# Kernel tuning notes

Hardware: AMD Instinct MI355X
Metric: run time of the kernel (lower is better)

The kernel has to match this reference:

```python
import jax, jax.numpy as jnp
import numpy as np

N, V, L = 256, 4, 100000
MUTATION_PROB = 0.2


def setup_inputs() -> dict:
    key = jax.random.key(0)
    k_s, k_mask, k_cat = jax.random.split(key, 3)
    # One-hot encoded input sequences (n, v, l), like the original module expects.
    base = jax.random.randint(k_s, (N, L), 0, V)
    s = jax.nn.one_hot(base, V, axis=1, dtype=jnp.float32)  # (n, v, l)
    # Externalized randomness: bernoulli mutation mask and uniform categorical draws.
    mask = jax.random.bernoulli(k_mask, MUTATION_PROB, (N, L))  # bool (n, l)
    cats = jax.random.randint(k_cat, (N, L), 0, V).astype(jnp.int32)  # (n, l)
    return {"s": s, "mask": mask, "cats": cats}


def reference(s, mask, cats):
    # s: (n, v, l) float; mask: (n, l) bool; cats: (n, l) int in [0, v)
    n, v, l = s.shape
    # One-hot of the sampled categories along the vocab axis -> (n, v, l)
    onehot = jax.nn.one_hot(cats, v, axis=1, dtype=s.dtype)
    # At mutated positions, replace the whole one-hot column with the new sample.
    return jnp.where(mask[:, None, :], onehot, s)
```

## Files before the change

kernel.cpp:

```cpp
#include <hip/hip_runtime.h>


#define N_SEQ 256
#define V_VOCAB 4
#define L_LEN 100000
#define L4 (L_LEN / 4)

__global__ void mutate_kernel(const float* __restrict__ s,
                              const int* __restrict__ mask,
                              const int* __restrict__ cats,
                              float* __restrict__ out) {
    const long long total = (long long)N_SEQ * L4;
    const long long stride = (long long)gridDim.x * blockDim.x;
    for (long long idx = (long long)blockIdx.x * blockDim.x + threadIdx.x;
         idx < total; idx += stride) {
        const int n  = (int)(idx / L4);
        const int lc = (int)(idx % L4);
        const long long nl = (long long)n * L_LEN + (long long)lc * 4;

        const int4 m = *reinterpret_cast<const int4*>(mask + nl);
        const int4 c = *reinterpret_cast<const int4*>(cats + nl);

        #pragma unroll
        for (int v = 0; v < V_VOCAB; ++v) {
            const long long off = ((long long)n * V_VOCAB + v) * L_LEN
                                + (long long)lc * 4;
            const float4 sv = *reinterpret_cast<const float4*>(s + off);
            float4 o;
            o.x = m.x ? (c.x == v ? 1.0f : 0.0f) : sv.x;
            o.y = m.y ? (c.y == v ? 1.0f : 0.0f) : sv.y;
            o.z = m.z ? (c.z == v ? 1.0f : 0.0f) : sv.z;
            o.w = m.w ? (c.w == v ? 1.0f : 0.0f) : sv.w;
            *reinterpret_cast<float4*>(out + off) = o;
        }
    }
}

extern "C" void kernel_launch(void* const* d_in, const int* in_sizes, int n_in,
                              void* d_out, int out_size, void* d_ws, size_t ws_size,
                              hipStream_t stream) {
    const float* s    = (const float*)d_in[0];
    const int*   mask = (const int*)d_in[1];
    const int*   cats = (const int*)d_in[2];
    float* out = (float*)d_out;

    const int block = 256;
    const long long total = (long long)N_SEQ * L4;
    int grid = (int)((total + block - 1) / block);
    if (grid > 2048) grid = 2048;

    mutate_kernel<<<grid, block, 0, stream>>>(s, mask, cats, out);
}
```

Before: 192.5 us.

## Use 2D grid, 8 elements per thread, and nontemporal loads/stores

Replaces the capped grid-stride loop with a 2D grid (chunks by sequence) so there is no per-element 64-bit div/mod. Each thread now handles 8 positions using two 16-byte vectors per stream, and all loads and stores use nontemporal hints to avoid polluting the cache with streaming data. This launches many more blocks and raises per-thread register use. Strided 32-byte per-thread accesses may reduce coalescing efficiency compared to contiguous 16-byte accesses.

Result: no change. 195.0 us (+1.3%).

```diff
diff --git a/kernel.cpp b/kernel.cpp
--- a/kernel.cpp
+++ b/kernel.cpp
@@ -4,35 +4,42 @@
 #define N_SEQ 256
 #define V_VOCAB 4
 #define L_LEN 100000
-#define L4 (L_LEN / 4)
+#define LPT 8
+#define L_CHUNKS (L_LEN / LPT)
 
-__global__ void mutate_kernel(const float* __restrict__ s,
-                              const int* __restrict__ mask,
-                              const int* __restrict__ cats,
-                              float* __restrict__ out) {
-    const long long total = (long long)N_SEQ * L4;
-    const long long stride = (long long)gridDim.x * blockDim.x;
-    for (long long idx = (long long)blockIdx.x * blockDim.x + threadIdx.x;
-         idx < total; idx += stride) {
-        const int n  = (int)(idx / L4);
-        const int lc = (int)(idx % L4);
-        const long long nl = (long long)n * L_LEN + (long long)lc * 4;
+typedef int   vint4   __attribute__((ext_vector_type(4)));
+typedef float vfloat4 __attribute__((ext_vector_type(4)));
 
-        const int4 m = *reinterpret_cast<const int4*>(mask + nl);
-        const int4 c = *reinterpret_cast<const int4*>(cats + nl);
+__global__ __launch_bounds__(256)
+void mutate_kernel(const float* __restrict__ s,
+                   const int* __restrict__ mask,
+                   const int* __restrict__ cats,
+                   float* __restrict__ out) {
+    const int lc = blockIdx.x * blockDim.x + threadIdx.x;
+    if (lc >= L_CHUNKS) return;
+    const int n = blockIdx.y;
 
+    const int l0 = lc * LPT;
+    const long long nl = (long long)n * L_LEN + l0;
+
+    const vint4 m0 = __builtin_nontemporal_load(reinterpret_cast<const vint4*>(mask + nl));
+    const vint4 m1 = __builtin_nontemporal_load(reinterpret_cast<const vint4*>(mask + nl) + 1);
+    const vint4 c0 = __builtin_nontemporal_load(reinterpret_cast<const vint4*>(cats + nl));
+    const vint4 c1 = __builtin_nontemporal_load(reinterpret_cast<const vint4*>(cats + nl) + 1);
+
+    #pragma unroll
+    for (int v = 0; v < V_VOCAB; ++v) {
+        const long long off = ((long long)n * V_VOCAB + v) * L_LEN + l0;
+        const vfloat4 s0 = __builtin_nontemporal_load(reinterpret_cast<const vfloat4*>(s + off));
+        const vfloat4 s1 = __builtin_nontemporal_load(reinterpret_cast<const vfloat4*>(s + off) + 1);
+        vfloat4 o0, o1;
         #pragma unroll
-        for (int v = 0; v < V_VOCAB; ++v) {
-            const long long off = ((long long)n * V_VOCAB + v) * L_LEN
-                                + (long long)lc * 4;
-            const float4 sv = *reinterpret_cast<const float4*>(s + off);
-            float4 o;
-            o.x = m.x ? (c.x == v ? 1.0f : 0.0f) : sv.x;
-            o.y = m.y ? (c.y == v ? 1.0f : 0.0f) : sv.y;
-            o.z = m.z ? (c.z == v ? 1.0f : 0.0f) : sv.z;
-            o.w = m.w ? (c.w == v ? 1.0f : 0.0f) : sv.w;
-            *reinterpret_cast<float4*>(out + off) = o;
+        for (int j = 0; j < 4; ++j) {
+            o0[j] = m0[j] ? (c0[j] == v ? 1.0f : 0.0f) : s0[j];
+            o1[j] = m1[j] ? (c1[j] == v ? 1.0f : 0.0f) : s1[j];
         }
+        __builtin_nontemporal_store(o0, reinterpret_cast<vfloat4*>(out + off));
+        __builtin_nontemporal_store(o1, reinterpret_cast<vfloat4*>(out + off) + 1);
     }
 }
 
@@ -45,9 +52,6 @@
     float* out = (float*)d_out;
 
     const int block = 256;
-    const long long total = (long long)N_SEQ * L4;
-    int grid = (int)((total + block - 1) / block);
-    if (grid > 2048) grid = 2048;
-
+    dim3 grid((L_CHUNKS + block - 1) / block, N_SEQ);
     mutate_kernel<<<grid, block, 0, stream>>>(s, mask, cats, out);
 }
```
